# Performance work log

Hardware: AMD Instinct MI355X
Metric: run time of the kernel (lower is better)

Reference implementation:

```python
import jax, jax.numpy as jnp
import numpy as np

C = 1024
RANK = 8


def _layernorm(x, g, b, eps=1e-5):
    mu = jnp.mean(x, axis=-1, keepdims=True)
    var = jnp.var(x, axis=-1, keepdims=True)
    return (x - mu) * jax.lax.rsqrt(var + eps) * g + b


def setup_inputs() -> dict:
    key = jax.random.key(0)
    ks = jax.random.split(key, 10)
    B, T = 4, 4096
    x = jax.random.normal(ks[0], (B, T, C), dtype=jnp.float32)
    # parameters (match torch inits)
    W0 = jnp.eye(C, dtype=jnp.float32) * 0.1
    A_init = jax.random.normal(ks[1], (C, RANK), dtype=jnp.float32) * 0.01
    B_init = jnp.zeros((RANK, C), dtype=jnp.float32)
    log_lr = jnp.full((C,), float(np.log(0.1)), dtype=jnp.float32)
    s = 1.0 / np.sqrt(C)
    Wq = jax.random.uniform(ks[2], (C, C), minval=-s, maxval=s, dtype=jnp.float32)
    Wk = jax.random.uniform(ks[3], (C, C), minval=-s, maxval=s, dtype=jnp.float32)
    Wv = jax.random.uniform(ks[4], (C, C), minval=-s, maxval=s, dtype=jnp.float32)
    Wo = jax.random.uniform(ks[5], (C, C), minval=-s, maxval=s, dtype=jnp.float32)
    Wg = jax.random.uniform(ks[6], (C, C), minval=-s, maxval=s, dtype=jnp.float32)
    ln_g = jnp.ones((C,), dtype=jnp.float32)
    ln_b = jnp.zeros((C,), dtype=jnp.float32)
    ls_g = jnp.full((C,), 1e-4, dtype=jnp.float32)  # LayerScale gamma
    return {"x": x, "W0": W0, "A_init": A_init, "B_init": B_init,
            "log_lr": log_lr, "Wq": Wq, "Wk": Wk, "Wv": Wv, "Wo": Wo,
            "Wg": Wg, "ln_g": ln_g, "ln_b": ln_b, "ls_g": ls_g}


def reference(x, W0, A_init, B_init, log_lr, Wq, Wk, Wv, Wo, Wg, ln_g, ln_b, ls_g):
    B, T, _ = x.shape
    h = _layernorm(x, ln_g, ln_b)
    # dual-form TTT (training path: q/k/v projections, full K @ W0)
    Q = jnp.einsum('btc,dc->btd', h, Wq)
    K = jnp.einsum('btc,dc->btd', h, Wk)
    V = jnp.einsum('btc,dc->btd', h, Wv)
    lr = jnp.minimum(jnp.exp(log_lr), 1.0)  # clamp(max=1.0)
    y0 = jnp.einsum('btc,cd->btd', K, W0) + jnp.einsum('btr,rd->btd', jnp.einsum('btc,cr->btr', K, A_init), B_init)
    error = y0 - V
    loss = jnp.mean(error ** 2)
    gradient = K * error                     # [B,T,C]
    grad_cumsum = jnp.cumsum(gradient, axis=1)
    grad_shift = jnp.concatenate([jnp.zeros((B, 1, gradient.shape[-1]), gradient.dtype), grad_cumsum[:, :-1, :]], axis=1)
    correction = Q * lr[None, None, :] * grad_shift
    pos = jnp.arange(1, T + 1, dtype=correction.dtype)
    pos_scale = (1.0 / (1.0 + 0.1 * jnp.log(pos)))[None, :, None]
    out = y0 - correction * pos_scale
    # gate, out projection, layer scale, residual
    gate = jax.nn.sigmoid(jnp.einsum('btc,dc->btd', x, Wg))
    out = out * gate
    out = jnp.einsum('btc,dc->btd', out, Wo) * ls_g
    return (x + out, loss)
```

## Files before the change

kernel.cpp:

```cpp
#include <hip/hip_runtime.h>
#include <stdint.h>
#include <math.h>

typedef unsigned short u16;
typedef __attribute__((ext_vector_type(8))) short short8;
typedef __attribute__((ext_vector_type(4))) float f32x4;

__device__ __forceinline__ float bf2f(u16 u){
  union { unsigned int i; float f; } v; v.i = ((unsigned int)u) << 16; return v.f;
}
__device__ __forceinline__ u16 f2bf(float f){
  union { float f; unsigned int i; } v; v.f = f;
  return (u16)((v.i + 0x7FFFu + ((v.i >> 16) & 1u)) >> 16);
}

__global__ void ln_prep(const float* __restrict__ x, const float* __restrict__ g,
                        const float* __restrict__ bta, u16* __restrict__ h,
                        u16* __restrict__ xb, float* __restrict__ loss){
  if (blockIdx.x == 0 && threadIdx.x == 0) loss[0] = 0.f;
  int row = blockIdx.x, tid = threadIdx.x;
  const float4* xr = (const float4*)(x + (size_t)row * 1024);
  float4 v = xr[tid];
  float s  = v.x + v.y + v.z + v.w;
  float s2 = v.x*v.x + v.y*v.y + v.z*v.z + v.w*v.w;
  #pragma unroll
  for (int o = 32; o > 0; o >>= 1){ s += __shfl_down(s, o); s2 += __shfl_down(s2, o); }
  __shared__ float red[8];
  if ((tid & 63) == 0){ red[tid >> 6] = s; red[4 + (tid >> 6)] = s2; }
  __syncthreads();
  float ts = red[0]+red[1]+red[2]+red[3];
  float t2 = red[4]+red[5]+red[6]+red[7];
  float mu   = ts * (1.0f/1024.0f);
  float var  = t2 * (1.0f/1024.0f) - mu*mu;
  float rstd = rsqrtf(var + 1e-5f);
  float4 gg = ((const float4*)g)[tid];
  float4 bb = ((const float4*)bta)[tid];
  ushort4 hv, xv;
  hv.x = f2bf((v.x-mu)*rstd*gg.x + bb.x);
  hv.y = f2bf((v.y-mu)*rstd*gg.y + bb.y);
  hv.z = f2bf((v.z-mu)*rstd*gg.z + bb.z);
  hv.w = f2bf((v.w-mu)*rstd*gg.w + bb.w);
  xv.x = f2bf(v.x); xv.y = f2bf(v.y); xv.z = f2bf(v.z); xv.w = f2bf(v.w);
  ((ushort4*)h )[(size_t)row*256 + tid] = hv;
  ((ushort4*)xb)[(size_t)row*256 + tid] = xv;
}

__global__ void prep_misc(const float* __restrict__ Wq, const float* __restrict__ Wk,
                          const float* __restrict__ Wv, const float* __restrict__ Wg,
                          const float* __restrict__ Wo, const float* __restrict__ W0,
                          const float* __restrict__ Ai, const float* __restrict__ Bi,
                          const float* __restrict__ llr,
                          u16* __restrict__ Wqb, u16* __restrict__ Wkb,
                          u16* __restrict__ Wvb, u16* __restrict__ Wgb,
                          u16* __restrict__ Wob, u16* __restrict__ Wet,
                          float* __restrict__ psg, float* __restrict__ lrc){
  int bx = blockIdx.x, tid = threadIdx.x;
  if (bx < 5120){
    int sel = bx >> 10;
    const float* s = sel==0?Wq : sel==1?Wk : sel==2?Wv : sel==3?Wg : Wo;
    u16* o = sel==0?Wqb : sel==1?Wkb : sel==2?Wvb : sel==3?Wgb : Wob;
    int i = (bx & 1023)*256 + tid;
    float4 v = ((const float4*)s)[i];
    ushort4 r; r.x=f2bf(v.x); r.y=f2bf(v.y); r.z=f2bf(v.z); r.w=f2bf(v.w);
    ((ushort4*)o)[i] = r;
  } else if (bx < 6144){
    __shared__ float tile[32][33];
    int wb = bx - 5120;
    int d0 = (wb & 31)*32, e0 = (wb >> 5)*32;
    int lr = tid >> 5, lc = tid & 31;
    #pragma unroll
    for (int s = 0; s < 4; ++s){
      int e = e0 + s*8 + lr, d = d0 + lc;
      float v = W0[(size_t)e*1024 + d];
      #pragma unroll
      for (int r = 0; r < 8; ++r) v += Ai[e*8 + r] * Bi[(size_t)r*1024 + d];
      tile[s*8 + lr][lc] = v;
    }
    __syncthreads();
    #pragma unroll
    for (int s = 0; s < 4; ++s){
      int d = d0 + s*8 + lr, e = e0 + lc;
      Wet[(size_t)d*1024 + e] = f2bf(tile[lc][s*8 + lr]);
    }
  } else {
    int t = (bx - 6144)*256 + tid;
    psg[t] = 1.0f/(1.0f + 0.1f*logf((float)(t+1)));
    if (t < 1024) lrc[t] = fminf(expf(llr[t]), 1.0f);
  }
}

template<int EPI>
__device__ __forceinline__ void gemm_body(const u16* __restrict__ A, const u16* __restrict__ Bm,
    u16* __restrict__ Cb, float* __restrict__ Cf, const float* __restrict__ lsg,
    const float* __restrict__ xres, int mblk, int nblk){
  __shared__ u16 smem[16384];
  u16* As = smem;
  u16* Bs = smem + 8192;
  const int tid  = threadIdx.x;
  const int lane = tid & 63;
  const int w    = tid >> 6;
  const int m0 = mblk * 128, n0 = nblk * 128;
  const int lrow = lane >> 3;
  const int gcol8 = (((lane & 7) ^ (lrow & 7)) * 8);
  const int wm = w & 1, wn = w >> 1;
  const int l15 = lane & 15, quad = lane >> 4;
  const int sw  = (l15 & 7);

  f32x4 acc[4][4] = {};

  #pragma unroll 1
  for (int kk = 0; kk < 1024; kk += 64){
    #pragma unroll
    for (int it = 0; it < 4; ++it){
      int r0 = w*8 + it*32;
      const u16* ga = A  + (size_t)(m0 + r0 + lrow)*1024 + kk + gcol8;
      __builtin_amdgcn_global_load_lds((const __attribute__((address_space(1))) unsigned int*)ga,
          (__attribute__((address_space(3))) unsigned int*)(As + r0*64), 16, 0, 0);
      const u16* gb = Bm + (size_t)(n0 + r0 + lrow)*1024 + kk + gcol8;
      __builtin_amdgcn_global_load_lds((const __attribute__((address_space(1))) unsigned int*)gb,
          (__attribute__((address_space(3))) unsigned int*)(Bs + r0*64), 16, 0, 0);
    }
    __syncthreads();
    #pragma unroll
    for (int kh = 0; kh < 2; ++kh){
      int kbi = kh*4 + quad;
      int koff = ((kbi ^ sw) * 8);
      short8 af[4], bfv[4];
      #pragma unroll
      for (int i = 0; i < 4; ++i) af[i]  = *(const short8*)(As + (wm*64 + i*16 + l15)*64 + koff);
      #pragma unroll
      for (int j = 0; j < 4; ++j) bfv[j] = *(const short8*)(Bs + (wn*64 + j*16 + l15)*64 + koff);
      #pragma unroll
      for (int i = 0; i < 4; ++i)
        #pragma unroll
        for (int j = 0; j < 4; ++j)
          acc[i][j] = __builtin_amdgcn_mfma_f32_16x16x32_bf16(af[i], bfv[j], acc[i][j], 0, 0, 0);
    }
    __syncthreads();
  }

  const int rbase = quad * 4;
  if (EPI == 0){
    #pragma unroll
    for (int i = 0; i < 4; ++i){
      int row = m0 + wm*64 + i*16 + rbase;
      #pragma unroll
      for (int j = 0; j < 4; ++j){
        int col = n0 + wn*64 + j*16 + l15;
        #pragma unroll
        for (int r = 0; r < 4; ++r)
          Cb[(size_t)(row + r)*1024 + col] = f2bf(acc[i][j][r]);
      }
    }
  } else {
    float* cf = (float*)smem;
    const int lr = tid >> 3, seg = tid & 7;
    float4 lsv[4];
    #pragma unroll
    for (int k = 0; k < 4; ++k) lsv[k] = *(const float4*)(lsg + n0 + seg*16 + k*4);
    #pragma unroll
    for (int i = 0; i < 4; ++i){
      __syncthreads();
      #pragma unroll
      for (int j = 0; j < 4; ++j)
        #pragma unroll
        for (int r = 0; r < 4; ++r)
          cf[(wm*16 + rbase + r)*132 + wn*64 + j*16 + l15] = acc[i][j][r];
      __syncthreads();
      int grow = m0 + i*16 + (lr & 15) + (lr >> 4)*64;
      size_t gbase = (size_t)grow*1024 + n0 + seg*16;
      #pragma unroll
      for (int k = 0; k < 4; ++k){
        float4 o = *(const float4*)(cf + lr*132 + seg*16 + k*4);
        float4 xr = *(const float4*)(xres + gbase + k*4);
        float4 res;
        res.x = o.x*lsv[k].x + xr.x; res.y = o.y*lsv[k].y + xr.y;
        res.z = o.z*lsv[k].z + xr.z; res.w = o.w*lsv[k].w + xr.w;
        *(float4*)(Cf + gbase + k*4) = res;
      }
    }
  }
}

__global__ void gemm_qkvg(const u16* __restrict__ h, const u16* __restrict__ xb,
                          const u16* __restrict__ Wqb, const u16* __restrict__ Wkb,
                          const u16* __restrict__ Wvb, const u16* __restrict__ Wgb,
                          u16* __restrict__ Qb, u16* __restrict__ Kb,
                          u16* __restrict__ Vb, u16* __restrict__ Gb){
  int sel = blockIdx.y >> 3;
  const u16* A  = (sel == 3) ? xb : h;
  const u16* Bm = sel==0?Wqb : sel==1?Wkb : sel==2?Wvb : Wgb;
  u16* Out      = sel==0?Qb  : sel==1?Kb  : sel==2?Vb  : Gb;
  gemm_body<0>(A, Bm, Out, nullptr, nullptr, nullptr, blockIdx.x, blockIdx.y & 7);
}

__global__ void gemm_y0(const u16* __restrict__ Kb, const u16* __restrict__ Wet,
                        u16* __restrict__ Yb){
  gemm_body<0>(Kb, Wet, Yb, nullptr, nullptr, nullptr, blockIdx.x, blockIdx.y);
}

__global__ void gemm_final(const u16* __restrict__ A, const u16* __restrict__ Bm,
                           float* __restrict__ C, const float* __restrict__ lsg,
                           const float* __restrict__ xres){
  gemm_body<1>(A, Bm, nullptr, C, lsg, xres, blockIdx.x, blockIdx.y);
}

__global__ void scan1(const u16* __restrict__ Kb, const u16* __restrict__ Vb,
                      const u16* __restrict__ Yb, u16* __restrict__ Gr,
                      float* __restrict__ part, float* __restrict__ loss){
  int tid = threadIdx.x;
  int c2  = blockIdx.x*128 + tid;
  int ch = blockIdx.y, b = blockIdx.z;
  size_t base = ((size_t)b*4096 + (size_t)ch*128)*512 + c2;
  const ushort2* K2 = (const ushort2*)Kb;
  const ushort2* V2 = (const ushort2*)Vb;
  const ushort2* Y2 = (const ushort2*)Yb;
  ushort2* G2 = (ushort2*)Gr;
  float g0 = 0.f, g1 = 0.f, ls = 0.f;
  #pragma unroll 8
  for (int t = 0; t < 128; ++t){
    size_t idx = base + (size_t)t*512;
    ushort2 kv = K2[idx], vv = V2[idx], yv = Y2[idx];
    float e0 = bf2f(yv.x) - bf2f(vv.x);
    float e1 = bf2f(yv.y) - bf2f(vv.y);
    float gv0 = bf2f(kv.x)*e0, gv1 = bf2f(kv.y)*e1;
    ushort2 gw; gw.x = f2bf(gv0); gw.y = f2bf(gv1);
    G2[idx] = gw;
    g0 += gv0; g1 += gv1; ls += e0*e0 + e1*e1;
  }
  float2 pw; pw.x = g0; pw.y = g1;
  *(float2*)(part + ((size_t)(b*32 + ch))*1024 + c2*2) = pw;
  #pragma unroll
  for (int o = 32; o > 0; o >>= 1) ls += __shfl_down(ls, o);
  __shared__ float red[2];
  if ((tid & 63) == 0) red[tid >> 6] = ls;
  __syncthreads();
  if (tid == 0) atomicAdd(loss, red[0] + red[1]);
}

__global__ void scan2(const u16* __restrict__ Gr, const u16* __restrict__ Yb,
                      const u16* __restrict__ Qb, const u16* __restrict__ Gb,
                      const float* __restrict__ part, const float* __restrict__ lrc,
                      const float* __restrict__ psg, u16* __restrict__ OutPre){
  int tid = threadIdx.x;
  int c2  = blockIdx.x*128 + tid;
  int ch = blockIdx.y, b = blockIdx.z;
  __shared__ float ps_s[128];
  ps_s[tid] = psg[ch*128 + tid];
  int c = c2*2;
  float run0 = 0.f, run1 = 0.f;
  for (int j = 0; j < ch; ++j){
    float2 pp = *(const float2*)(part + ((size_t)(b*32 + j))*1024 + c);
    run0 += pp.x; run1 += pp.y;
  }
  float2 lr2 = *(const float2*)(lrc + c);
  __syncthreads();
  size_t base = ((size_t)b*4096 + (size_t)ch*128)*512 + c2;
  const ushort2* Gr2 = (const ushort2*)Gr;
  const ushort2* Yb2 = (const ushort2*)Yb;
  const ushort2* Qb2 = (const ushort2*)Qb;
  const ushort2* Gb2 = (const ushort2*)Gb;
  ushort2* Ot2 = (ushort2*)OutPre;
  #pragma unroll 8
  for (int t = 0; t < 128; ++t){
    size_t idx = base + (size_t)t*512;
    ushort2 gr = Gr2[idx], yv = Yb2[idx], qv = Qb2[idx], gl = Gb2[idx];
    float ps = ps_s[t];
    float g0 = 1.0f/(1.0f + expf(-bf2f(gl.x)));
    float g1 = 1.0f/(1.0f + expf(-bf2f(gl.y)));
    float o0 = (bf2f(yv.x) - bf2f(qv.x)*lr2.x*run0*ps) * g0;
    float o1 = (bf2f(yv.y) - bf2f(qv.y)*lr2.y*run1*ps) * g1;
    ushort2 ov; ov.x = f2bf(o0); ov.y = f2bf(o1);
    Ot2[idx] = ov;
    run0 += bf2f(gr.x); run1 += bf2f(gr.y);
  }
}

__global__ void finloss(const float* __restrict__ loss, float* __restrict__ o){
  o[0] = loss[0] * (1.0f/16777216.0f);
}

extern "C" void kernel_launch(void* const* d_in, const int* in_sizes, int n_in,
                              void* d_out, int out_size, void* d_ws, size_t ws_size,
                              hipStream_t stream){
  const float* x   = (const float*)d_in[0];
  const float* W0  = (const float*)d_in[1];
  const float* Ai  = (const float*)d_in[2];
  const float* Bi  = (const float*)d_in[3];
  const float* llr = (const float*)d_in[4];
  const float* Wq  = (const float*)d_in[5];
  const float* Wk  = (const float*)d_in[6];
  const float* Wv  = (const float*)d_in[7];
  const float* Wo  = (const float*)d_in[8];
  const float* Wg  = (const float*)d_in[9];
  const float* lng = (const float*)d_in[10];
  const float* lnb = (const float*)d_in[11];
  const float* lsg = (const float*)d_in[12];
  float* out = (float*)d_out;

  const size_t TOK = 16384, CC = 1024;
  char* p = (char*)d_ws;
  float* loss = (float*)p; p += 256;
  u16* h   = (u16*)p; p += TOK*CC*2;
  u16* xb  = (u16*)p; p += TOK*CC*2;
  u16* Qb  = (u16*)p; p += TOK*CC*2;
  u16* Kb  = (u16*)p; p += TOK*CC*2;
  u16* Vb  = (u16*)p; p += TOK*CC*2;
  u16* Gb  = (u16*)p; p += TOK*CC*2;
  u16* Wqb = (u16*)p; p += CC*CC*2;
  u16* Wkb = (u16*)p; p += CC*CC*2;
  u16* Wvb = (u16*)p; p += CC*CC*2;
  u16* Wgb = (u16*)p; p += CC*CC*2;
  u16* Wob = (u16*)p; p += CC*CC*2;
  u16* Wet = (u16*)p; p += CC*CC*2;
  float* psg  = (float*)p; p += 4096*4;
  float* lrc  = (float*)p; p += 1024*4;
  float* part = (float*)p; p += (size_t)128*1024*4;

  ln_prep<<<16384, 256, 0, stream>>>(x, lng, lnb, h, xb, loss);
  prep_misc<<<6160, 256, 0, stream>>>(Wq, Wk, Wv, Wg, Wo, W0, Ai, Bi, llr,
                                      Wqb, Wkb, Wvb, Wgb, Wob, Wet, psg, lrc);
  gemm_qkvg<<<dim3(128, 32), 256, 0, stream>>>(h, xb, Wqb, Wkb, Wvb, Wgb, Qb, Kb, Vb, Gb);
  gemm_y0<<<dim3(128, 8), 256, 0, stream>>>(Kb, Wet, h);
  scan1<<<dim3(4, 32, 4), 128, 0, stream>>>(Kb, Vb, h, xb, part, loss);
  scan2<<<dim3(4, 32, 4), 128, 0, stream>>>(xb, h, Qb, Gb, part, lrc, psg, Qb);
  gemm_final<<<dim3(128, 8), 256, 0, stream>>>(Qb, Wob, out, lsg, x);
  finloss<<<1, 1, 0, stream>>>(loss, out + 16777216);
}
```

Before: 517.9 us.

## Merge prep kernels, reorder GEMM block mapping, halve scan chunk size, fold loss

Merges the layernorm and weight-conversion prep kernels into one launch and folds the final loss scaling into the output GEMM, removing two kernel launches. The GEMM grids are flattened so consecutive blocks share the same M tile across N tiles, which may improve L2 reuse of the A operand. The scan kernels now use 64-token chunks instead of 128, doubling the number of blocks for more parallelism, at the cost of a larger partial-sum buffer and longer prefix loops in scan2.

```diff
diff --git a/kernel.cpp b/kernel.cpp
--- a/kernel.cpp
+++ b/kernel.cpp
@@ -14,58 +14,58 @@
   return (u16)((v.i + 0x7FFFu + ((v.i >> 16) & 1u)) >> 16);
 }
 
-__global__ void ln_prep(const float* __restrict__ x, const float* __restrict__ g,
-                        const float* __restrict__ bta, u16* __restrict__ h,
-                        u16* __restrict__ xb, float* __restrict__ loss){
-  if (blockIdx.x == 0 && threadIdx.x == 0) loss[0] = 0.f;
-  int row = blockIdx.x, tid = threadIdx.x;
-  const float4* xr = (const float4*)(x + (size_t)row * 1024);
-  float4 v = xr[tid];
-  float s  = v.x + v.y + v.z + v.w;
-  float s2 = v.x*v.x + v.y*v.y + v.z*v.z + v.w*v.w;
-  #pragma unroll
-  for (int o = 32; o > 0; o >>= 1){ s += __shfl_down(s, o); s2 += __shfl_down(s2, o); }
-  __shared__ float red[8];
-  if ((tid & 63) == 0){ red[tid >> 6] = s; red[4 + (tid >> 6)] = s2; }
-  __syncthreads();
-  float ts = red[0]+red[1]+red[2]+red[3];
-  float t2 = red[4]+red[5]+red[6]+red[7];
-  float mu   = ts * (1.0f/1024.0f);
-  float var  = t2 * (1.0f/1024.0f) - mu*mu;
-  float rstd = rsqrtf(var + 1e-5f);
-  float4 gg = ((const float4*)g)[tid];
-  float4 bb = ((const float4*)bta)[tid];
-  ushort4 hv, xv;
-  hv.x = f2bf((v.x-mu)*rstd*gg.x + bb.x);
-  hv.y = f2bf((v.y-mu)*rstd*gg.y + bb.y);
-  hv.z = f2bf((v.z-mu)*rstd*gg.z + bb.z);
-  hv.w = f2bf((v.w-mu)*rstd*gg.w + bb.w);
-  xv.x = f2bf(v.x); xv.y = f2bf(v.y); xv.z = f2bf(v.z); xv.w = f2bf(v.w);
-  ((ushort4*)h )[(size_t)row*256 + tid] = hv;
-  ((ushort4*)xb)[(size_t)row*256 + tid] = xv;
-}
-
-__global__ void prep_misc(const float* __restrict__ Wq, const float* __restrict__ Wk,
-                          const float* __restrict__ Wv, const float* __restrict__ Wg,
-                          const float* __restrict__ Wo, const float* __restrict__ W0,
-                          const float* __restrict__ Ai, const float* __restrict__ Bi,
-                          const float* __restrict__ llr,
-                          u16* __restrict__ Wqb, u16* __restrict__ Wkb,
-                          u16* __restrict__ Wvb, u16* __restrict__ Wgb,
-                          u16* __restrict__ Wob, u16* __restrict__ Wet,
-                          float* __restrict__ psg, float* __restrict__ lrc){
+__global__ void prep_all(const float* __restrict__ x, const float* __restrict__ lng,
+                         const float* __restrict__ lnb,
+                         const float* __restrict__ Wq, const float* __restrict__ Wk,
+                         const float* __restrict__ Wv, const float* __restrict__ Wg,
+                         const float* __restrict__ Wo, const float* __restrict__ W0,
+                         const float* __restrict__ Ai, const float* __restrict__ Bi,
+                         const float* __restrict__ llr,
+                         u16* __restrict__ h, u16* __restrict__ xb,
+                         u16* __restrict__ Wqb, u16* __restrict__ Wkb,
+                         u16* __restrict__ Wvb, u16* __restrict__ Wgb,
+                         u16* __restrict__ Wob, u16* __restrict__ Wet,
+                         float* __restrict__ psg, float* __restrict__ lrc,
+                         float* __restrict__ loss){
   int bx = blockIdx.x, tid = threadIdx.x;
-  if (bx < 5120){
-    int sel = bx >> 10;
+  if (bx < 16384){
+    if (bx == 0 && tid == 0) loss[0] = 0.f;
+    int row = bx;
+    float4 v = ((const float4*)(x + (size_t)row * 1024))[tid];
+    float s  = v.x + v.y + v.z + v.w;
+    float s2 = v.x*v.x + v.y*v.y + v.z*v.z + v.w*v.w;
+    #pragma unroll
+    for (int o = 32; o > 0; o >>= 1){ s += __shfl_down(s, o); s2 += __shfl_down(s2, o); }
+    __shared__ float red[8];
+    if ((tid & 63) == 0){ red[tid >> 6] = s; red[4 + (tid >> 6)] = s2; }
+    __syncthreads();
+    float ts = red[0]+red[1]+red[2]+red[3];
+    float t2 = red[4]+red[5]+red[6]+red[7];
+    float mu   = ts * (1.0f/1024.0f);
+    float var  = t2 * (1.0f/1024.0f) - mu*mu;
+    float rstd = rsqrtf(var + 1e-5f);
+    float4 gg = ((const float4*)lng)[tid];
+    float4 bb = ((const float4*)lnb)[tid];
+    ushort4 hv, xv;
+    hv.x = f2bf((v.x-mu)*rstd*gg.x + bb.x);
+    hv.y = f2bf((v.y-mu)*rstd*gg.y + bb.y);
+    hv.z = f2bf((v.z-mu)*rstd*gg.z + bb.z);
+    hv.w = f2bf((v.w-mu)*rstd*gg.w + bb.w);
+    xv.x = f2bf(v.x); xv.y = f2bf(v.y); xv.z = f2bf(v.z); xv.w = f2bf(v.w);
+    ((ushort4*)h )[(size_t)row*256 + tid] = hv;
+    ((ushort4*)xb)[(size_t)row*256 + tid] = xv;
+  } else if (bx < 21504){
+    int cb = bx - 16384;
+    int sel = cb >> 10;
     const float* s = sel==0?Wq : sel==1?Wk : sel==2?Wv : sel==3?Wg : Wo;
     u16* o = sel==0?Wqb : sel==1?Wkb : sel==2?Wvb : sel==3?Wgb : Wob;
-    int i = (bx & 1023)*256 + tid;
+    int i = (cb & 1023)*256 + tid;
     float4 v = ((const float4*)s)[i];
     ushort4 r; r.x=f2bf(v.x); r.y=f2bf(v.y); r.z=f2bf(v.z); r.w=f2bf(v.w);
     ((ushort4*)o)[i] = r;
-  } else if (bx < 6144){
+  } else if (bx < 22528){
     __shared__ float tile[32][33];
-    int wb = bx - 5120;
+    int wb = bx - 21504;
     int d0 = (wb & 31)*32, e0 = (wb >> 5)*32;
     int lr = tid >> 5, lc = tid & 31;
     #pragma unroll
@@ -83,7 +83,7 @@
       Wet[(size_t)d*1024 + e] = f2bf(tile[lc][s*8 + lr]);
     }
   } else {
-    int t = (bx - 6144)*256 + tid;
+    int t = (bx - 22528)*256 + tid;
     psg[t] = 1.0f/(1.0f + 0.1f*logf((float)(t+1)));
     if (t < 1024) lrc[t] = fminf(expf(llr[t]), 1.0f);
   }
@@ -187,22 +187,27 @@
                           const u16* __restrict__ Wvb, const u16* __restrict__ Wgb,
                           u16* __restrict__ Qb, u16* __restrict__ Kb,
                           u16* __restrict__ Vb, u16* __restrict__ Gb){
-  int sel = blockIdx.y >> 3;
+  int bid = blockIdx.x;
+  int mblk = bid >> 5, sub = bid & 31;
+  int sel = sub >> 3, nblk = sub & 7;
   const u16* A  = (sel == 3) ? xb : h;
   const u16* Bm = sel==0?Wqb : sel==1?Wkb : sel==2?Wvb : Wgb;
   u16* Out      = sel==0?Qb  : sel==1?Kb  : sel==2?Vb  : Gb;
-  gemm_body<0>(A, Bm, Out, nullptr, nullptr, nullptr, blockIdx.x, blockIdx.y & 7);
+  gemm_body<0>(A, Bm, Out, nullptr, nullptr, nullptr, mblk, nblk);
 }
 
 __global__ void gemm_y0(const u16* __restrict__ Kb, const u16* __restrict__ Wet,
                         u16* __restrict__ Yb){
-  gemm_body<0>(Kb, Wet, Yb, nullptr, nullptr, nullptr, blockIdx.x, blockIdx.y);
+  int bid = blockIdx.x;
+  gemm_body<0>(Kb, Wet, Yb, nullptr, nullptr, nullptr, bid >> 3, bid & 7);
 }
 
 __global__ void gemm_final(const u16* __restrict__ A, const u16* __restrict__ Bm,
                            float* __restrict__ C, const float* __restrict__ lsg,
-                           const float* __restrict__ xres){
-  gemm_body<1>(A, Bm, nullptr, C, lsg, xres, blockIdx.x, blockIdx.y);
+                           const float* __restrict__ xres, const float* __restrict__ loss){
+  int bid = blockIdx.x;
+  if (bid == 0 && threadIdx.x == 0) C[16777216] = loss[0] * (1.0f/16777216.0f);
+  gemm_body<1>(A, Bm, nullptr, C, lsg, xres, bid >> 3, bid & 7);
 }
 
 __global__ void scan1(const u16* __restrict__ Kb, const u16* __restrict__ Vb,
@@ -211,14 +216,14 @@
   int tid = threadIdx.x;
   int c2  = blockIdx.x*128 + tid;
   int ch = blockIdx.y, b = blockIdx.z;
-  size_t base = ((size_t)b*4096 + (size_t)ch*128)*512 + c2;
+  size_t base = ((size_t)b*4096 + (size_t)ch*64)*512 + c2;
   const ushort2* K2 = (const ushort2*)Kb;
   const ushort2* V2 = (const ushort2*)Vb;
   const ushort2* Y2 = (const ushort2*)Yb;
   ushort2* G2 = (ushort2*)Gr;
   float g0 = 0.f, g1 = 0.f, ls = 0.f;
   #pragma unroll 8
-  for (int t = 0; t < 128; ++t){
+  for (int t = 0; t < 64; ++t){
     size_t idx = base + (size_t)t*512;
     ushort2 kv = K2[idx], vv = V2[idx], yv = Y2[idx];
     float e0 = bf2f(yv.x) - bf2f(vv.x);
@@ -229,7 +234,7 @@
     g0 += gv0; g1 += gv1; ls += e0*e0 + e1*e1;
   }
   float2 pw; pw.x = g0; pw.y = g1;
-  *(float2*)(part + ((size_t)(b*32 + ch))*1024 + c2*2) = pw;
+  *(float2*)(part + ((size_t)(b*64 + ch))*1024 + c2*2) = pw;
   #pragma unroll
   for (int o = 32; o > 0; o >>= 1) ls += __shfl_down(ls, o);
   __shared__ float red[2];
@@ -245,24 +250,24 @@
   int tid = threadIdx.x;
   int c2  = blockIdx.x*128 + tid;
   int ch = blockIdx.y, b = blockIdx.z;
-  __shared__ float ps_s[128];
-  ps_s[tid] = psg[ch*128 + tid];
+  __shared__ float ps_s[64];
+  if (tid < 64) ps_s[tid] = psg[ch*64 + tid];
   int c = c2*2;
   float run0 = 0.f, run1 = 0.f;
   for (int j = 0; j < ch; ++j){
-    float2 pp = *(const float2*)(part + ((size_t)(b*32 + j))*1024 + c);
+    float2 pp = *(const float2*)(part + ((size_t)(b*64 + j))*1024 + c);
     run0 += pp.x; run1 += pp.y;
   }
   float2 lr2 = *(const float2*)(lrc + c);
   __syncthreads();
-  size_t base = ((size_t)b*4096 + (size_t)ch*128)*512 + c2;
+  size_t base = ((size_t)b*4096 + (size_t)ch*64)*512 + c2;
   const ushort2* Gr2 = (const ushort2*)Gr;
   const ushort2* Yb2 = (const ushort2*)Yb;
   const ushort2* Qb2 = (const ushort2*)Qb;
   const ushort2* Gb2 = (const ushort2*)Gb;
   ushort2* Ot2 = (ushort2*)OutPre;
   #pragma unroll 8
-  for (int t = 0; t < 128; ++t){
+  for (int t = 0; t < 64; ++t){
     size_t idx = base + (size_t)t*512;
     ushort2 gr = Gr2[idx], yv = Yb2[idx], qv = Qb2[idx], gl = Gb2[idx];
     float ps = ps_s[t];
@@ -274,10 +279,6 @@
     Ot2[idx] = ov;
     run0 += bf2f(gr.x); run1 += bf2f(gr.y);
   }
-}
-
-__global__ void finloss(const float* __restrict__ loss, float* __restrict__ o){
-  o[0] = loss[0] * (1.0f/16777216.0f);
 }
 
 extern "C" void kernel_launch(void* const* d_in, const int* in_sizes, int n_in,
@@ -315,15 +316,13 @@
   u16* Wet = (u16*)p; p += CC*CC*2;
   float* psg  = (float*)p; p += 4096*4;
   float* lrc  = (float*)p; p += 1024*4;
-  float* part = (float*)p; p += (size_t)128*1024*4;
-
-  ln_prep<<<16384, 256, 0, stream>>>(x, lng, lnb, h, xb, loss);
-  prep_misc<<<6160, 256, 0, stream>>>(Wq, Wk, Wv, Wg, Wo, W0, Ai, Bi, llr,
-                                      Wqb, Wkb, Wvb, Wgb, Wob, Wet, psg, lrc);
-  gemm_qkvg<<<dim3(128, 32), 256, 0, stream>>>(h, xb, Wqb, Wkb, Wvb, Wgb, Qb, Kb, Vb, Gb);
-  gemm_y0<<<dim3(128, 8), 256, 0, stream>>>(Kb, Wet, h);
-  scan1<<<dim3(4, 32, 4), 128, 0, stream>>>(Kb, Vb, h, xb, part, loss);
-  scan2<<<dim3(4, 32, 4), 128, 0, stream>>>(xb, h, Qb, Gb, part, lrc, psg, Qb);
-  gemm_final<<<dim3(128, 8), 256, 0, stream>>>(Qb, Wob, out, lsg, x);
-  finloss<<<1, 1, 0, stream>>>(loss, out + 16777216);
-}
+  float* part = (float*)p; p += (size_t)256*1024*4;
+
+  prep_all<<<22544, 256, 0, stream>>>(x, lng, lnb, Wq, Wk, Wv, Wg, Wo, W0, Ai, Bi, llr,
+                                      h, xb, Wqb, Wkb, Wvb, Wgb, Wob, Wet, psg, lrc, loss);
+  gemm_qkvg<<<4096, 256, 0, stream>>>(h, xb, Wqb, Wkb, Wvb, Wgb, Qb, Kb, Vb, Gb);
+  gemm_y0<<<1024, 256, 0, stream>>>(Kb, Wet, h);
+  scan1<<<dim3(4, 64, 4), 128, 0, stream>>>(Kb, Vb, h, xb, part, loss);
+  scan2<<<dim3(4, 64, 4), 128, 0, stream>>>(xb, h, Qb, Gb, part, lrc, psg, Qb);
+  gemm_final<<<1024, 256, 0, stream>>>(Qb, Wob, out, lsg, x, loss);
+}
```

Measured after the change: 514.9 us. No clear change (-0.6%).
